# Kernel tuning notes

Measured on AMD Instinct MI355X. Metric: run time of the kernel, lower is better.

## Reference

```python
import jax, jax.numpy as jnp
import numpy as np

WH, WW = 12, 12          # window size
NUM_HEADS = 12
DIM = 384
CPB_HIDDEN = 512


def _relative_coords_table():
    # (1, 2*Wh-1, 2*Ww-1, 2), log-scaled continuous relative coords (pretrained_window_size == 0 path)
    ch = np.arange(-(WH - 1), WH, dtype=np.float32)
    cw = np.arange(-(WW - 1), WW, dtype=np.float32)
    t = np.stack(np.meshgrid(ch, cw, indexing='ij'), axis=-1)[None]  # (1, 2Wh-1, 2Ww-1, 2)
    t = t.copy()
    t[..., 0] /= (WH - 1)
    t[..., 1] /= (WW - 1)
    t = t * 8.0
    t = np.sign(t) * np.log2(np.abs(t) + 1.0) / np.log2(8.0)
    return jnp.asarray(t, dtype=jnp.float32)


def _relative_position_index():
    ch = np.arange(WH)
    cw = np.arange(WW)
    coords = np.stack(np.meshgrid(ch, cw, indexing='ij'))          # (2, Wh, Ww)
    cf = coords.reshape(2, -1)                                      # (2, N)
    rel = (cf[:, :, None] - cf[:, None, :]).transpose(1, 2, 0)      # (N, N, 2)
    rel[..., 0] += WH - 1
    rel[..., 1] += WW - 1
    rel[..., 0] *= 2 * WW - 1
    return jnp.asarray(rel.sum(-1), dtype=jnp.int32)                # (N, N)


def _l2_normalize(x):
    rnorm = jax.lax.rsqrt(jnp.maximum(jnp.sum(x * x, axis=-1, keepdims=True), 1e-12))
    return x * rnorm


def setup_inputs() -> dict:
    key = jax.random.key(0)
    ks = jax.random.split(key, 10)
    B_, N, C = 512, WH * WW, DIM
    s = lambda fan_in: 1.0 / np.sqrt(fan_in)
    return {
        'x': jax.random.normal(ks[0], (B_, N, C), dtype=jnp.float32),
        'w_qkv': jax.random.normal(ks[1], (C, 3 * C), dtype=jnp.float32) * s(C),
        'q_bias': jnp.zeros((C,), dtype=jnp.float32),
        'v_bias': jnp.zeros((C,), dtype=jnp.float32),
        'logit_scale': jnp.log(10.0 * jnp.ones((NUM_HEADS, 1, 1), dtype=jnp.float32)),
        'cpb_w1': jax.random.normal(ks[2], (2, CPB_HIDDEN), dtype=jnp.float32) * s(2),
        'cpb_b1': jnp.zeros((CPB_HIDDEN,), dtype=jnp.float32),
        'cpb_w2': jax.random.normal(ks[3], (CPB_HIDDEN, NUM_HEADS), dtype=jnp.float32) * s(CPB_HIDDEN),
        'proj_w': jax.random.normal(ks[4], (C, C), dtype=jnp.float32) * s(C),
        'proj_b': jnp.zeros((C,), dtype=jnp.float32),
    }


def reference(x, w_qkv, q_bias, v_bias, logit_scale, cpb_w1, cpb_b1, cpb_w2, proj_w, proj_b):
    B_, N, C = x.shape
    H = NUM_HEADS
    Dh = C // H

    # qkv projection (no bias in Dense) + manual qkv bias with zero k-bias
    qkv_bias = jnp.concatenate([q_bias, jnp.zeros_like(v_bias), v_bias])
    qkv = x @ w_qkv + qkv_bias                                  # (B_, N, 3C)
    qkv = qkv.reshape(B_, N, 3, H, Dh).transpose(2, 0, 3, 1, 4)  # (3, B_, H, N, Dh)
    q, k, v = qkv[0], qkv[1], qkv[2]

    # cosine attention with learnable clamped temperature
    qn = _l2_normalize(q)
    kn = _l2_normalize(k)
    scale = jnp.exp(jnp.minimum(logit_scale, np.log(100.0)))     # (H, 1, 1)
    attn = jnp.einsum('bhnd,bhmd->bhnm', qn, kn) * scale         # (B_, H, N, N)

    # continuous position bias (CPB) MLP over the relative coords table
    table = _relative_coords_table()                             # (1, 2Wh-1, 2Ww-1, 2)
    bias_table = jnp.maximum(table @ cpb_w1 + cpb_b1, 0.0) @ cpb_w2   # (1, 2Wh-1, 2Ww-1, H)
    bias_table = bias_table.reshape(-1, H)                       # ((2Wh-1)*(2Ww-1), H)
    rpi = _relative_position_index().reshape(-1)                 # (N*N,)
    rel_bias = bias_table[rpi].reshape(N, N, H).transpose(2, 0, 1)  # (H, N, N)
    rel_bias = 16.0 * jax.nn.sigmoid(rel_bias)
    attn = attn + rel_bias[None]                                 # broadcast over B_

    attn = jax.nn.softmax(attn, axis=-1)
    out = jnp.einsum('bhnm,bhmd->bhnd', attn, v)                 # (B_, H, N, Dh)
    out = out.transpose(0, 2, 1, 3).reshape(B_, N, C)
    return out @ proj_w + proj_b
```

## Files before the change

### kernel.cpp

```cpp
#include <hip/hip_runtime.h>
#include <hip/hip_bf16.h>
#include <cstdint>
#include <cstddef>

typedef __attribute__((ext_vector_type(8))) short short8;
typedef __attribute__((ext_vector_type(4))) float f32x4;

__device__ __forceinline__ float b2f(ushort u) {
  union { float f; uint32_t i; } x; x.i = ((uint32_t)u) << 16; return x.f;
}
__device__ __forceinline__ ushort f2b(float f) {
  uint32_t i = __builtin_bit_cast(uint32_t, f);
  i += 0x7fffu + ((i >> 16) & 1u);
  return (ushort)(i >> 16);
}
__device__ __forceinline__ f32x4 mfma16(short8 a, short8 b, f32x4 c) {
  asm("v_mfma_f32_16x16x32_bf16 %0, %1, %2, %0" : "+v"(c) : "v"(a), "v"(b));
  return c;
}
__device__ __forceinline__ void gload_lds16(const void* g, void* l) {
  auto gp = reinterpret_cast<const __attribute__((address_space(1))) uint32_t*>(
      reinterpret_cast<uintptr_t>(g));
  auto lp = reinterpret_cast<__attribute__((address_space(3))) uint32_t*>(
      reinterpret_cast<uintptr_t>(l));
  __builtin_amdgcn_global_load_lds(gp, lp, 16, 0, 0);
}

__global__ __launch_bounds__(256) void k_cvtx(const float* __restrict__ x, ushort* __restrict__ o) {
  size_t i = (size_t)blockIdx.x * 256 + threadIdx.x;
  const float4* xp = (const float4*)x;
  float4 a = xp[i * 2], b = xp[i * 2 + 1];
  union { short8 v; ushort u[8]; } r;
  r.u[0] = f2b(a.x); r.u[1] = f2b(a.y); r.u[2] = f2b(a.z); r.u[3] = f2b(a.w);
  r.u[4] = f2b(b.x); r.u[5] = f2b(b.y); r.u[6] = f2b(b.z); r.u[7] = f2b(b.w);
  *(short8*)&o[i * 8] = r.v;
}

__global__ __launch_bounds__(256) void k_cvtT(const float* __restrict__ W, ushort* __restrict__ Wt,
                                              int R, int C) {
  int r = blockIdx.x;
  for (int c = threadIdx.x; c < C; c += 256)
    Wt[(size_t)c * R + r] = f2b(W[(size_t)r * C + c]);
}

__device__ __forceinline__ float cpb_coord(int i) {
  float v = (float)(i - 11) * (8.0f / 11.0f);
  float l = log2f(fabsf(v) + 1.0f) * (1.0f / 3.0f);
  return v < 0.0f ? -l : l;
}

__global__ void k_cpb1(const float* __restrict__ w1, const float* __restrict__ b1,
                       const float* __restrict__ w2, float* __restrict__ bt) {
  int e = blockIdx.x;
  float t0 = cpb_coord(e / 23);
  float t1 = cpb_coord(e % 23);
  float acc[12];
#pragma unroll
  for (int h = 0; h < 12; h++) acc[h] = 0.0f;
  for (int u = threadIdx.x; u < 512; u += 64) {
    float hv = fmaxf(fmaf(t0, w1[u], fmaf(t1, w1[512 + u], b1[u])), 0.0f);
#pragma unroll
    for (int h = 0; h < 12; h++) acc[h] = fmaf(hv, w2[u * 12 + h], acc[h]);
  }
#pragma unroll
  for (int h = 0; h < 12; h++)
    for (int m = 1; m < 64; m <<= 1) acc[h] += __shfl_xor(acc[h], m);
  if (threadIdx.x == 0) {
#pragma unroll
    for (int h = 0; h < 12; h++) bt[e * 12 + h] = acc[h];
  }
}

__global__ void k_cpb2(const float* __restrict__ bt, float* __restrict__ rb) {
  int h = blockIdx.x / 144, i = blockIdx.x % 144;
  int j = threadIdx.x;
  if (j >= 144) return;
  int yi = i / 12, xi = i % 12, yj = j / 12, xj = j % 12;
  int idx = (yi - yj + 11) * 23 + (xi - xj + 11);
  float v = bt[idx * 12 + h];
  rb[((size_t)h * 144 + i) * 144 + j] = 16.0f / (1.0f + expf(-v));
}

template <int EPI>
__global__ __launch_bounds__(256) void k_gemm(
    const ushort* __restrict__ A, const ushort* __restrict__ Bt, int K, int NB,
    const float* __restrict__ bias0, const float* __restrict__ bias1,
    ushort* __restrict__ O0, ushort* __restrict__ O1, ushort* __restrict__ O2,
    float* __restrict__ FO) {
  __shared__ __align__(16) ushort Smem[2 * 128 * 64];
  ushort* As = Smem;
  ushort* Bs = Smem + 128 * 64;
  const int tid = threadIdx.x;
  const int lane = tid & 63, w = tid >> 6;
  const int wr = w >> 1, wc = w & 1;
  const int l15 = lane & 15, g = lane >> 4;

  const int per = gridDim.x >> 3;
  const int bid = (blockIdx.x & 7) * per + (blockIdx.x >> 3);
  const int bm = bid / NB, bn = bid % NB;

  f32x4 acc[4][4];
#pragma unroll
  for (int m = 0; m < 4; m++)
#pragma unroll
    for (int n = 0; n < 4; n++) acc[m][n] = (f32x4){0.f, 0.f, 0.f, 0.f};

  const size_t arow0 = (size_t)bm * 128;
  const size_t brow0 = (size_t)bn * 128;

  const int srow = lane >> 3;
  const int sblk0 = (lane & 7) ^ srow;
  const size_t soff = (size_t)srow * K + sblk0 * 8;

  for (int k0 = 0; k0 < K; k0 += 64) {
#pragma unroll
    for (int i = 0; i < 4; i++) {
      int c = i * 4 + w;
      gload_lds16(&A[(arow0 + c * 8) * (size_t)K + k0 + soff], &As[c * 512]);
      gload_lds16(&Bt[(brow0 + c * 8) * (size_t)K + k0 + soff], &Bs[c * 512]);
    }
    __syncthreads();
#pragma unroll
    for (int ks = 0; ks < 2; ks++) {
      short8 af[4], bf[4];
#pragma unroll
      for (int m = 0; m < 4; m++) {
        int row = wr * 64 + m * 16 + l15;
        af[m] = *(const short8*)&As[row * 64 + (((ks * 4 + g) ^ (row & 7)) << 3)];
      }
#pragma unroll
      for (int n = 0; n < 4; n++) {
        int row = wc * 64 + n * 16 + l15;
        bf[n] = *(const short8*)&Bs[row * 64 + (((ks * 4 + g) ^ (row & 7)) << 3)];
      }
#pragma unroll
      for (int m = 0; m < 4; m++)
#pragma unroll
        for (int n = 0; n < 4; n++) acc[m][n] = mfma16(af[m], bf[n], acc[m][n]);
    }
    __syncthreads();
  }

  unsigned char* Cb = (unsigned char*)Smem;

  if (EPI == 0) {
    const int sec = bn / 3;
    const int cbase = (bn - sec * 3) * 128;
    if (sec == 2) {
      float vb4[4];
#pragma unroll
      for (int n = 0; n < 4; n++) vb4[n] = bias1[cbase + wc * 64 + n * 16 + l15];
#pragma unroll
      for (int m = 0; m < 4; m++) {
        int rbase = bm * 128 + wr * 64 + m * 16 + g * 4;
        int b = rbase / 144, nn = rbase - b * 144;
#pragma unroll
        for (int n = 0; n < 4; n++) {
          int cc = cbase + wc * 64 + n * 16 + l15;
          int head = cc >> 5, d = cc & 31;
          ushort4 pk;
          pk.x = f2b(acc[m][n][0] + vb4[n]);
          pk.y = f2b(acc[m][n][1] + vb4[n]);
          pk.z = f2b(acc[m][n][2] + vb4[n]);
          pk.w = f2b(acc[m][n][3] + vb4[n]);
          *(ushort4*)&O2[(((size_t)b * 12 + head) * 32 + d) * 144 + nn] = pk;
        }
      }
    } else {
      float bn4[4];
#pragma unroll
      for (int n = 0; n < 4; n++)
        bn4[n] = (sec == 0) ? bias0[cbase + wc * 64 + n * 16 + l15] : 0.0f;
#pragma unroll
      for (int m = 0; m < 4; m++)
#pragma unroll
        for (int n = 0; n < 4; n++) {
          int col = wc * 64 + n * 16 + l15;
#pragma unroll
          for (int e = 0; e < 4; e++) {
            int row = wr * 64 + m * 16 + g * 4 + e;
            int sblk = (col >> 3) ^ ((row >> 2) & 7);
            *(ushort*)&Cb[row * 256 + sblk * 16 + (col & 7) * 2] =
                f2b(acc[m][n][e] + bn4[n]);
          }
        }
      __syncthreads();
      int r = tid >> 1, half = tid & 1;
      int grow = bm * 128 + r;
      int b = grow / 144, nn = grow - b * 144;
      ushort* dst = (sec == 0) ? O0 : O1;
#pragma unroll
      for (int j = 0; j < 8; j++) {
        int lb = half * 8 + j;
        int sblk = lb ^ ((r >> 2) & 7);
        uint4 v = *(uint4*)&Cb[r * 256 + sblk * 16];
        int c0 = cbase + lb * 8;
        int head = c0 >> 5, d0 = c0 & 31;
        *(uint4*)&dst[(((size_t)b * 12 + head) * 144 + nn) * 32 + d0] = v;
      }
    }
  } else {
    float bn4[4];
#pragma unroll
    for (int n = 0; n < 4; n++) bn4[n] = bias0[bn * 128 + wc * 64 + n * 16 + l15];
#pragma unroll
    for (int p = 0; p < 2; p++) {
      if (wc == p) {
#pragma unroll
        for (int m = 0; m < 4; m++)
#pragma unroll
          for (int n = 0; n < 4; n++) {
            int lcol = n * 16 + l15;
#pragma unroll
            for (int e = 0; e < 4; e++) {
              int row = wr * 64 + m * 16 + g * 4 + e;
              int sblk = (lcol >> 2) ^ ((row >> 2) & 7);
              *(float*)&Cb[row * 256 + sblk * 16 + (lcol & 3) * 4] =
                  acc[m][n][e] + bn4[n];
            }
          }
      }
      __syncthreads();
      int r = tid >> 1, half = tid & 1;
#pragma unroll
      for (int j = 0; j < 8; j++) {
        int lb = half * 8 + j;
        int sblk = lb ^ ((r >> 2) & 7);
        uint4 v = *(uint4*)&Cb[r * 256 + sblk * 16];
        *(uint4*)&FO[(size_t)(bm * 128 + r) * 384 + bn * 128 + p * 64 + lb * 4] = v;
      }
      __syncthreads();
    }
  }
}

__global__ __launch_bounds__(256, 3) void k_attn(
    const ushort* __restrict__ Qg, const ushort* __restrict__ Kg, const ushort* __restrict__ VTg,
    const float* __restrict__ lsc, const float* __restrict__ relb, ushort* __restrict__ AO) {
  __shared__ ushort Qs[144 * 32];
  __shared__ ushort Ks[144 * 32];
  __shared__ ushort Vt[32 * 168];
  __shared__ ushort Pw[4][16 * 168];
  __shared__ float rq[144], rk[144];

  const int tid = threadIdx.x;
  const int lane = tid & 63, w = tid >> 6;
  const int l15 = lane & 15, g = lane >> 4;
  const int bh = blockIdx.x;
  const int b = bh / 12, h = bh % 12;
  const size_t base = (size_t)bh * 4608;

  for (int f = tid; f < 576; f += 256) {
    int row = f >> 2, oct = f & 3;
    union { uint4 v; ushort u[8]; } qv, kv;
    qv.v = *(const uint4*)&Qg[base + row * 32 + oct * 8];
    kv.v = *(const uint4*)&Kg[base + row * 32 + oct * 8];
    int blk = (oct ^ (row & 3)) << 3;
    *(uint4*)&Qs[row * 32 + blk] = qv.v;
    *(uint4*)&Ks[row * 32 + blk] = kv.v;
    float sq = 0.f, sk = 0.f;
#pragma unroll
    for (int j = 0; j < 8; j++) {
      float xq = b2f(qv.u[j]); sq = fmaf(xq, xq, sq);
      float xk = b2f(kv.u[j]); sk = fmaf(xk, xk, sk);
    }
    sq += __shfl_xor(sq, 1); sq += __shfl_xor(sq, 2);
    sk += __shfl_xor(sk, 1); sk += __shfl_xor(sk, 2);
    if (oct == 0) {
      rq[row] = rsqrtf(fmaxf(sq, 1e-12f));
      rk[row] = rsqrtf(fmaxf(sk, 1e-12f));
    }
  }
  for (int f = tid; f < 576; f += 256) {
    int d = f / 18, j = f % 18;
    *(uint4*)&Vt[d * 168 + j * 8] = *(const uint4*)&VTg[base + d * 144 + j * 8];
  }
  if (tid < 64) {
    int d = tid >> 1, j = tid & 1;
    *(uint4*)&Vt[d * 168 + 144 + j * 8] = (uint4){0, 0, 0, 0};
  }
  if (lane < 32) {
    int r = lane >> 1, j = lane & 1;
    *(uint4*)&Pw[w][r * 168 + 144 + j * 8] = (uint4){0, 0, 0, 0};
  }
  __syncthreads();

  short8 kf[9];
  f32x4 rk4[9];
#pragma unroll
  for (int tj = 0; tj < 9; tj++) {
    int R = tj * 16 + l15;
    kf[tj] = *(const short8*)&Ks[R * 32 + ((g ^ (R & 3)) << 3)];
    rk4[tj] = *(const f32x4*)&rk[tj * 16 + g * 4];
  }

  const float sc = __expf(fminf(lsc[h], 4.6051702f));
  const float shift = sc + 16.0f;
  const float* rbh = relb + (size_t)h * (144 * 144);

  for (int ti = w; ti < 9; ti += 4) {
    int RQ = ti * 16 + l15;
    short8 aq = *(const short8*)&Qs[RQ * 32 + ((g ^ (RQ & 3)) << 3)];
    f32x4 s[9];
#pragma unroll
    for (int tj = 0; tj < 9; tj++) {
      f32x4 z = {0.f, 0.f, 0.f, 0.f};
      s[tj] = mfma16(kf[tj], aq, z);
    }
    const float rq_l = rq[RQ] * sc;
    const float* rbq = rbh + (size_t)RQ * 144;

    float lg[9][4];
    float ssum = 0.f;
#pragma unroll
    for (int tj = 0; tj < 9; tj++) {
      f32x4 rbv = *(const f32x4*)&rbq[tj * 16 + g * 4];
#pragma unroll
      for (int e = 0; e < 4; e++) {
        float v = fmaf(s[tj][e] * rq_l, rk4[tj][e], rbv[e]);
        v = __expf(v - shift);
        lg[tj][e] = v;
        ssum += v;
      }
    }
    ssum += __shfl_xor(ssum, 16);
    ssum += __shfl_xor(ssum, 32);
    const float inv = 1.0f / ssum;

#pragma unroll
    for (int tj = 0; tj < 9; tj++) {
      ushort4 pk;
      pk.x = f2b(lg[tj][0] * inv);
      pk.y = f2b(lg[tj][1] * inv);
      pk.z = f2b(lg[tj][2] * inv);
      pk.w = f2b(lg[tj][3] * inv);
      *(ushort4*)&Pw[w][l15 * 168 + tj * 16 + g * 4] = pk;
    }

    asm volatile("s_waitcnt lgkmcnt(0)" ::: "memory");
    __builtin_amdgcn_sched_barrier(0);

#pragma unroll
    for (int dt = 0; dt < 2; dt++) {
      f32x4 o = {0.f, 0.f, 0.f, 0.f};
#pragma unroll
      for (int ks = 0; ks < 5; ks++) {
        short8 ap = *(const short8*)&Pw[w][l15 * 168 + ks * 32 + g * 8];
        short8 bv = *(const short8*)&Vt[(dt * 16 + l15) * 168 + ks * 32 + g * 8];
        o = mfma16(ap, bv, o);
      }
      ushort* dst = &AO[((size_t)b * 144 + ti * 16 + g * 4) * 384 + h * 32 + dt * 16 + l15];
#pragma unroll
      for (int e = 0; e < 4; e++) dst[(size_t)e * 384] = f2b(o[e]);
    }
  }
}

extern "C" void kernel_launch(void* const* d_in, const int* in_sizes, int n_in,
                              void* d_out, int out_size, void* d_ws, size_t ws_size,
                              hipStream_t stream) {
  const float* x     = (const float*)d_in[0];
  const float* wqkv  = (const float*)d_in[1];
  const float* qbias = (const float*)d_in[2];
  const float* vbias = (const float*)d_in[3];
  const float* lsc   = (const float*)d_in[4];
  const float* cw1   = (const float*)d_in[5];
  const float* cb1   = (const float*)d_in[6];
  const float* cw2   = (const float*)d_in[7];
  const float* pw    = (const float*)d_in[8];
  const float* pb    = (const float*)d_in[9];

  char* ws = (char*)d_ws;
  ushort* xb = (ushort*)(ws);
  ushort* wt = (ushort*)(ws + 56623104);
  ushort* pt = (ushort*)(ws + 57507840);
  ushort* qb = (ushort*)(ws + 57802752);
  ushort* kb = (ushort*)(ws + 114425856);
  ushort* vb = (ushort*)(ws + 171048960);
  float*  bt = (float*)(ws + 227672064);
  float*  rb = (float*)(ws + 227697456);
  ushort* ao = xb;

  k_cvtx<<<13824, 256, 0, stream>>>(x, xb);
  k_cvtT<<<384, 256, 0, stream>>>(wqkv, wt, 384, 1152);
  k_cvtT<<<384, 256, 0, stream>>>(pw, pt, 384, 384);
  k_cpb1<<<529, 64, 0, stream>>>(cw1, cb1, cw2, bt);
  k_cpb2<<<1728, 144, 0, stream>>>(bt, rb);
  k_gemm<0><<<5184, 256, 0, stream>>>(xb, wt, 384, 9, qbias, vbias, qb, kb, vb, nullptr);
  k_attn<<<6144, 256, 0, stream>>>(qb, kb, vb, lsc, rb, ao);
  k_gemm<1><<<1728, 256, 0, stream>>>(ao, pt, 384, 3, pb, nullptr, nullptr, nullptr, nullptr, (float*)d_out);
}
```

Measured before the change: 284.3 us.

## Double-buffer GEMM LDS tiles with K-step 32 to overlap loads and MFMA

The GEMM main loop now uses two LDS buffers, each with a K-tile of 32 instead of a single K-tile of 64. The global-to-LDS load for the next tile is issued before computing on the current tile, so memory traffic overlaps with MFMA work and one barrier per iteration is removed. The LDS swizzle is redone for the 32-wide rows. In exchange there are twice as many loop iterations and less MFMA work per barrier. Correctness relies on the async direct-to-LDS loads having completed by the single __syncthreads.

```diff
diff --git a/kernel.cpp b/kernel.cpp
--- a/kernel.cpp
+++ b/kernel.cpp
@@ -87,9 +87,7 @@
     const float* __restrict__ bias0, const float* __restrict__ bias1,
     ushort* __restrict__ O0, ushort* __restrict__ O1, ushort* __restrict__ O2,
     float* __restrict__ FO) {
-  __shared__ __align__(16) ushort Smem[2 * 128 * 64];
-  ushort* As = Smem;
-  ushort* Bs = Smem + 128 * 64;
+  __shared__ __align__(16) ushort Smem[2 * 2 * 128 * 32];
   const int tid = threadIdx.x;
   const int lane = tid & 63, w = tid >> 6;
   const int wr = w >> 1, wc = w & 1;
@@ -108,38 +106,49 @@
   const size_t arow0 = (size_t)bm * 128;
   const size_t brow0 = (size_t)bn * 128;
 
-  const int srow = lane >> 3;
-  const int sblk0 = (lane & 7) ^ srow;
-  const size_t soff = (size_t)srow * K + sblk0 * 8;
-
-  for (int k0 = 0; k0 < K; k0 += 64) {
-#pragma unroll
-    for (int i = 0; i < 4; i++) {
-      int c = i * 4 + w;
-      gload_lds16(&A[(arow0 + c * 8) * (size_t)K + k0 + soff], &As[c * 512]);
-      gload_lds16(&Bt[(brow0 + c * 8) * (size_t)K + k0 + soff], &Bs[c * 512]);
-    }
+  const int srow = lane >> 2;
+  const int sblk = (lane & 3) ^ ((srow >> 1) & 3);
+  const size_t soff = (size_t)srow * K + sblk * 8;
+
+#define GEMM_STAGE(BUF, K0)                                                      \
+  do {                                                                           \
+    ushort* As_ = &Smem[(BUF) * 8192];                                           \
+    ushort* Bs_ = &Smem[(BUF) * 8192 + 4096];                                    \
+    _Pragma("unroll")                                                            \
+    for (int i_ = 0; i_ < 2; i_++) {                                             \
+      int c_ = w * 2 + i_;                                                       \
+      gload_lds16(&A[(arow0 + c_ * 16) * (size_t)K + (K0) + soff], &As_[c_ * 512]); \
+      gload_lds16(&Bt[(brow0 + c_ * 16) * (size_t)K + (K0) + soff], &Bs_[c_ * 512]);\
+    }                                                                            \
+  } while (0)
+
+  GEMM_STAGE(0, 0);
+  __syncthreads();
+
+  int cur = 0;
+  for (int k0 = 0; k0 < K; k0 += 32) {
+    if (k0 + 32 < K) GEMM_STAGE(cur ^ 1, k0 + 32);
+    const ushort* As = &Smem[cur * 8192];
+    const ushort* Bs = &Smem[cur * 8192 + 4096];
+    short8 af[4], bf[4];
+#pragma unroll
+    for (int m = 0; m < 4; m++) {
+      int row = wr * 64 + m * 16 + l15;
+      af[m] = *(const short8*)&As[row * 32 + ((g ^ ((row >> 1) & 3)) << 3)];
+    }
+#pragma unroll
+    for (int n = 0; n < 4; n++) {
+      int row = wc * 64 + n * 16 + l15;
+      bf[n] = *(const short8*)&Bs[row * 32 + ((g ^ ((row >> 1) & 3)) << 3)];
+    }
+#pragma unroll
+    for (int m = 0; m < 4; m++)
+#pragma unroll
+      for (int n = 0; n < 4; n++) acc[m][n] = mfma16(af[m], bf[n], acc[m][n]);
     __syncthreads();
-#pragma unroll
-    for (int ks = 0; ks < 2; ks++) {
-      short8 af[4], bf[4];
-#pragma unroll
-      for (int m = 0; m < 4; m++) {
-        int row = wr * 64 + m * 16 + l15;
-        af[m] = *(const short8*)&As[row * 64 + (((ks * 4 + g) ^ (row & 7)) << 3)];
-      }
-#pragma unroll
-      for (int n = 0; n < 4; n++) {
-        int row = wc * 64 + n * 16 + l15;
-        bf[n] = *(const short8*)&Bs[row * 64 + (((ks * 4 + g) ^ (row & 7)) << 3)];
-      }
-#pragma unroll
-      for (int m = 0; m < 4; m++)
-#pragma unroll
-        for (int n = 0; n < 4; n++) acc[m][n] = mfma16(af[m], bf[n], acc[m][n]);
-    }
-    __syncthreads();
-  }
+    cur ^= 1;
+  }
+#undef GEMM_STAGE
 
   unsigned char* Cb = (unsigned char*)Smem;
 
@@ -179,8 +188,8 @@
 #pragma unroll
           for (int e = 0; e < 4; e++) {
             int row = wr * 64 + m * 16 + g * 4 + e;
-            int sblk = (col >> 3) ^ ((row >> 2) & 7);
-            *(ushort*)&Cb[row * 256 + sblk * 16 + (col & 7) * 2] =
+            int sblk2 = (col >> 3) ^ ((row >> 2) & 7);
+            *(ushort*)&Cb[row * 256 + sblk2 * 16 + (col & 7) * 2] =
                 f2b(acc[m][n][e] + bn4[n]);
           }
         }
@@ -192,8 +201,8 @@
 #pragma unroll
       for (int j = 0; j < 8; j++) {
         int lb = half * 8 + j;
-        int sblk = lb ^ ((r >> 2) & 7);
-        uint4 v = *(uint4*)&Cb[r * 256 + sblk * 16];
+        int sblk2 = lb ^ ((r >> 2) & 7);
+        uint4 v = *(uint4*)&Cb[r * 256 + sblk2 * 16];
         int c0 = cbase + lb * 8;
         int head = c0 >> 5, d0 = c0 & 31;
         *(uint4*)&dst[(((size_t)b * 12 + head) * 144 + nn) * 32 + d0] = v;
@@ -214,8 +223,8 @@
 #pragma unroll
             for (int e = 0; e < 4; e++) {
               int row = wr * 64 + m * 16 + g * 4 + e;
-              int sblk = (lcol >> 2) ^ ((row >> 2) & 7);
-              *(float*)&Cb[row * 256 + sblk * 16 + (lcol & 3) * 4] =
+              int sblk2 = (lcol >> 2) ^ ((row >> 2) & 7);
+              *(float*)&Cb[row * 256 + sblk2 * 16 + (lcol & 3) * 4] =
                   acc[m][n][e] + bn4[n];
             }
           }
@@ -225,8 +234,8 @@
 #pragma unroll
       for (int j = 0; j < 8; j++) {
         int lb = half * 8 + j;
-        int sblk = lb ^ ((r >> 2) & 7);
-        uint4 v = *(uint4*)&Cb[r * 256 + sblk * 16];
+        int sblk2 = lb ^ ((r >> 2) & 7);
+        uint4 v = *(uint4*)&Cb[r * 256 + sblk2 * 16];
         *(uint4*)&FO[(size_t)(bm * 128 + r) * 384 + bn * 128 + p * 64 + lb * 4] = v;
       }
       __syncthreads();
```

Result: slower. 292.4 us (+2.8%).
